# Kernel tuning notes

Measured on AMD Instinct MI355X. Metric: run time of the kernel, lower is better.

## Reference

```python
import jax, jax.numpy as jnp
import numpy as np

H, C = 8, 32          # heads, per-head channels
N, E = 100000, 1600000
NEG_SLOPE = 0.2
LN_EPS = 1e-5


def layer_norm(x, g, b):
    mu = jnp.mean(x, axis=-1, keepdims=True)
    var = jnp.mean((x - mu) ** 2, axis=-1, keepdims=True)
    return (x - mu) * jax.lax.rsqrt(var + LN_EPS) * g + b


def setup_inputs() -> dict:
    key = jax.random.key(0)
    ks = jax.random.split(key, 8)
    x = jax.random.normal(ks[0], (N, C), dtype=jnp.float32)
    edge_index = jax.random.randint(ks[1], (2, E), 0, N, dtype=jnp.int64)
    s = 1.0 / np.sqrt(C)
    W_gat = jax.random.normal(ks[2], (C, H * C), dtype=jnp.float32) * s
    att_src = jax.random.normal(ks[3], (H, C), dtype=jnp.float32) * s
    att_dst = jax.random.normal(ks[4], (H, C), dtype=jnp.float32) * s
    bias_gat = jnp.zeros((C,), jnp.float32)
    w1 = jax.random.normal(ks[5], (C, 128), dtype=jnp.float32) * s
    b1 = jnp.zeros((128,), jnp.float32)
    w2 = jax.random.normal(ks[6], (128, C), dtype=jnp.float32) / np.sqrt(128)
    b2 = jnp.zeros((C,), jnp.float32)
    g1 = jnp.ones((C,), jnp.float32); be1 = jnp.zeros((C,), jnp.float32)
    g2 = jnp.ones((C,), jnp.float32); be2 = jnp.zeros((C,), jnp.float32)
    return dict(x=x, edge_index=edge_index, W_gat=W_gat, att_src=att_src,
                att_dst=att_dst, bias_gat=bias_gat, w1=w1, b1=b1, w2=w2,
                b2=b2, g1=g1, be1=be1, g2=g2, be2=be2)


def gat_conv(x, edge_index, W_gat, att_src, att_dst, bias_gat):
    n = x.shape[0]
    # add self loops (PyG default)
    loops = jnp.arange(n, dtype=edge_index.dtype)
    ei = jnp.concatenate([edge_index, jnp.stack([loops, loops])], axis=1)
    src, dst = ei[0], ei[1]
    xp = (x @ W_gat).reshape(n, H, C)                      # [N,H,C]
    a_src = jnp.einsum('nhc,hc->nh', xp, att_src)          # [N,H]
    a_dst = jnp.einsum('nhc,hc->nh', xp, att_dst)
    alpha = jax.nn.leaky_relu(a_src[src] + a_dst[dst], NEG_SLOPE)  # [E',H]
    # segment softmax over incoming edges of each dst node
    m = jax.ops.segment_max(alpha, dst, num_segments=n)
    ea = jnp.exp(alpha - m[dst])
    denom = jax.ops.segment_sum(ea, dst, num_segments=n)
    attn = ea / (denom[dst] + 1e-16)                       # [E',H]
    msg = xp[src] * attn[..., None]                        # [E',H,C]
    out = jax.ops.segment_sum(msg, dst, num_segments=n)    # [N,H,C]
    return out.mean(axis=1) + bias_gat                     # concat=False -> head mean


def reference(x, edge_index, W_gat, att_src, att_dst, bias_gat,
              w1, b1, w2, b2, g1, be1, g2, be2):
    h = gat_conv(x, edge_index, W_gat, att_src, att_dst, bias_gat)
    h = layer_norm(h + x, g1, be1)
    ff = jax.nn.relu(h @ w1 + b1) @ w2 + b2
    return layer_norm(ff + h, g2, be2)
```

## Files before the change

### kernel.cpp

```cpp
#include <hip/hip_runtime.h>
#include <hip/hip_fp16.h>
#include <stdint.h>

#define HH 8
#define CC 32
#define HC 256
#define FF 128
#define NEG 0.2f
#define LNEPS 1e-5f

typedef __attribute__((ext_vector_type(8))) short bf16x8;
typedef __attribute__((ext_vector_type(4))) float f32x4;
typedef unsigned short u16;

__device__ inline unsigned bf16r(float f) {
  unsigned u = __float_as_uint(f);
  return (u + 0x7fffu + ((u >> 16) & 1u)) >> 16;
}
__device__ inline float bflo(unsigned w) { return __uint_as_float(w << 16); }
__device__ inline float bfhi(unsigned w) { return __uint_as_float(w & 0xffff0000u); }
__device__ inline float leaky(float v) { return v >= 0.f ? v : NEG * v; }
__device__ inline float h2f(unsigned hbits) {
  return __half2float(__ushort_as_half((unsigned short)hbits));
}
__device__ inline u16 f2h(float f) {
  return __half_as_ushort(__float2half(f));
}
__device__ inline float ub0(unsigned w) { return (float)(w & 0xffu); }
__device__ inline float ub1(unsigned w) { return (float)((w >> 8) & 0xffu); }
__device__ inline float ub2(unsigned w) { return (float)((w >> 16) & 0xffu); }
__device__ inline float ub3(unsigned w) { return (float)(w >> 24); }

__global__ __launch_bounds__(256) void klayout(
    const float* __restrict__ W, const float* __restrict__ atts,
    const float* __restrict__ attd, const float* __restrict__ w1,
    const float* __restrict__ w2,
    u16* __restrict__ Wb, u16* __restrict__ Zb,
    u16* __restrict__ V1b, u16* __restrict__ V2b, u16* __restrict__ WSb)
{
  int t0 = (int)blockIdx.x * 256 + (int)threadIdx.x;
  int st = (int)gridDim.x * 256;
  for (int i = t0; i < 16 * 512; i += st) {
    int j = i & 7, l = (i >> 3) & 63, nb = i >> 9;
    int k = 8 * (l >> 4) + j, c = 16 * nb + (l & 15);
    Wb[i] = (u16)bf16r(W[k * HC + c]);
  }
  for (int i = t0; i < 8 * 512; i += st) {
    int j = i & 7, l = (i >> 3) & 63, kb = i >> 9;
    int k = 32 * kb + 8 * (l >> 4) + j;
    int tc = l & 15;
    float v = 0.f;
    if (tc < 8)  { if ((k >> 5) == tc)     v = atts[tc * 32 + (k & 31)]; }
    else         { if ((k >> 5) == tc - 8) v = attd[(tc - 8) * 32 + (k & 31)]; }
    Zb[i] = (u16)bf16r(v);
  }
  for (int i = t0; i < 8 * 512; i += st) {
    int j = i & 7, l = (i >> 3) & 63, nb = i >> 9;
    int k = 8 * (l >> 4) + j, c = 16 * nb + (l & 15);
    V1b[i] = (u16)bf16r(w1[k * FF + c]);
  }
  for (int i = t0; i < 8 * 512; i += st) {
    int j = i & 7, l = (i >> 3) & 63, kn = i >> 9;
    int kb = kn >> 1, nb2 = kn & 1;
    int k = 32 * kb + 8 * (l >> 4) + j, c = 16 * nb2 + (l & 15);
    V2b[i] = (u16)bf16r(w2[k * CC + c]);
  }
  for (int i = t0; i < 16 * 512; i += st) {
    int j = i & 7, l = (i >> 3) & 63, kn = i >> 9;
    int kb = kn >> 1, nb2 = kn & 1;
    int krow = kb * 32 + 8 * (l >> 4) + j;
    int h = krow >> 5, kk = krow & 31;
    int c = 16 * nb2 + (l & 15);
    WSb[i] = (u16)bf16r(W[kk * HC + h * 32 + c]);
  }
}

__global__ __launch_bounds__(256) void k1c(
    const float* __restrict__ x, const u16* __restrict__ Wb,
    const u16* __restrict__ Zb, const int* __restrict__ ei,
    unsigned* __restrict__ xqx, unsigned* __restrict__ ascp,
    float* __restrict__ a_d, int* __restrict__ deg4,
    unsigned* __restrict__ dstr, int n, int e, int nbc)
{
  if ((int)blockIdx.x >= nbc) {
    int bi = (int)blockIdx.x - nbc;
    int r = bi & 3;
    int* dr = deg4 + (size_t)r * n;
    int i = bi * 1024 + (int)threadIdx.x * 4;
    if (i >= e) return;
    const int* dst = ei + e;
    if (i + 3 < e) {
      int4 d4 = *(const int4*)(dst + i);
      unsigned r0 = (unsigned)atomicAdd(&dr[d4.x], 1);
      unsigned r1 = (unsigned)atomicAdd(&dr[d4.y], 1);
      unsigned r2 = (unsigned)atomicAdd(&dr[d4.z], 1);
      unsigned r3 = (unsigned)atomicAdd(&dr[d4.w], 1);
      uint4 o;
      o.x = (unsigned)d4.x | ((unsigned)r << 17) | (r0 << 19);
      o.y = (unsigned)d4.y | ((unsigned)r << 17) | (r1 << 19);
      o.z = (unsigned)d4.z | ((unsigned)r << 17) | (r2 << 19);
      o.w = (unsigned)d4.w | ((unsigned)r << 17) | (r3 << 19);
      *(uint4*)(dstr + i) = o;
    } else {
      for (int k = 0; k < 4 && i + k < e; ++k) {
        int d = dst[i + k];
        unsigned rr = (unsigned)atomicAdd(&dr[d], 1);
        dstr[i + k] = (unsigned)d | ((unsigned)r << 17) | (rr << 19);
      }
    }
    return;
  }
  __shared__ u16 lt[4][16 * 264];
  int wid = threadIdx.x >> 6, lane = threadIdx.x & 63;
  int q = lane & 15, g = lane >> 4;
  long node0 = (long)((int)blockIdx.x * 4 + wid) * 16;
  if (node0 + 16 > n) node0 = n - 16;
  u16* L = lt[wid];
  u16* ascp16 = (u16*)ascp;

  const float* xr = x + (node0 + q) * CC + 8 * g;
  float4 xa = *(const float4*)xr, xb = *(const float4*)(xr + 4);
  bf16x8 af;
  af[0] = (short)bf16r(xa.x); af[1] = (short)bf16r(xa.y);
  af[2] = (short)bf16r(xa.z); af[3] = (short)bf16r(xa.w);
  af[4] = (short)bf16r(xb.x); af[5] = (short)bf16r(xb.y);
  af[6] = (short)bf16r(xb.z); af[7] = (short)bf16r(xb.w);

  float mx = fmaxf(fmaxf(fmaxf(fabsf(xa.x), fabsf(xa.y)), fmaxf(fabsf(xa.z), fabsf(xa.w))),
                   fmaxf(fmaxf(fabsf(xb.x), fabsf(xb.y)), fmaxf(fabsf(xb.z), fabsf(xb.w))));
  mx = fmaxf(mx, __shfl_xor(mx, 16));
  mx = fmaxf(mx, __shfl_xor(mx, 32));
  float rinv = (mx > 0.f) ? 127.f / mx : 0.f;
  u16 sch = f2h(mx * (1.f / 127.f));
  ascp16[((node0 + q) * HH + 2 * g) * 2 + 1]     = sch;
  ascp16[((node0 + q) * HH + 2 * g + 1) * 2 + 1] = sch;
  {
    int q0 = min(max(__float2int_rn(xa.x * rinv), -127), 127) + 128;
    int q1 = min(max(__float2int_rn(xa.y * rinv), -127), 127) + 128;
    int q2 = min(max(__float2int_rn(xa.z * rinv), -127), 127) + 128;
    int q3 = min(max(__float2int_rn(xa.w * rinv), -127), 127) + 128;
    int q4 = min(max(__float2int_rn(xb.x * rinv), -127), 127) + 128;
    int q5 = min(max(__float2int_rn(xb.y * rinv), -127), 127) + 128;
    int q6 = min(max(__float2int_rn(xb.z * rinv), -127), 127) + 128;
    int q7 = min(max(__float2int_rn(xb.w * rinv), -127), 127) + 128;
    uint2 pk;
    pk.x = (unsigned)q0 | ((unsigned)q1 << 8) | ((unsigned)q2 << 16) | ((unsigned)q3 << 24);
    pk.y = (unsigned)q4 | ((unsigned)q5 << 8) | ((unsigned)q6 << 16) | ((unsigned)q7 << 24);
    *(uint2*)(xqx + (node0 + q) * 8 + 2 * g) = pk;
  }

#pragma unroll
  for (int nb = 0; nb < 16; ++nb) {
    bf16x8 bf = *(const bf16x8*)(Wb + nb * 512 + lane * 8);
    f32x4 acc = {0.f, 0.f, 0.f, 0.f};
    acc = __builtin_amdgcn_mfma_f32_16x16x32_bf16(af, bf, acc, 0, 0, 0);
    int col = 16 * nb + q;
#pragma unroll
    for (int r = 0; r < 4; ++r)
      L[(4 * g + r) * 264 + col] = (u16)bf16r(acc[r]);
  }
  __syncthreads();

  f32x4 az = {0.f, 0.f, 0.f, 0.f};
#pragma unroll
  for (int kb = 0; kb < 8; ++kb) {
    bf16x8 a2 = *(const bf16x8*)(L + q * 264 + kb * 32 + g * 8);
    bf16x8 zb = *(const bf16x8*)(Zb + kb * 512 + lane * 8);
    az = __builtin_amdgcn_mfma_f32_16x16x32_bf16(a2, zb, az, 0, 0, 0);
  }
  int hq = q & 7;
  if (q < 8) {
#pragma unroll
    for (int r = 0; r < 4; ++r)
      ascp16[((node0 + 4 * g + r) * HH + hq) * 2] = (u16)bf16r(az[r]);
  } else {
#pragma unroll
    for (int r = 0; r < 4; ++r)
      a_d[(node0 + 4 * g + r) * HH + hq] = az[r];
  }
}

__global__ __launch_bounds__(256) void kscanA(const int* __restrict__ deg4,
                                              int* __restrict__ bsum, int n)
{
  __shared__ int ws[4];
  int t = threadIdx.x;
  int i = (int)blockIdx.x * 1024 + t * 4;
  int s = 0;
  if (i + 3 < n) {
#pragma unroll
    for (int r = 0; r < 4; ++r) {
      int4 v = *(const int4*)(deg4 + (size_t)r * n + i);
      s += v.x + v.y + v.z + v.w;
    }
  } else {
    for (int k = 0; k < 4 && i + k < n; ++k)
#pragma unroll
      for (int r = 0; r < 4; ++r) s += deg4[(size_t)r * n + i + k];
  }
#pragma unroll
  for (int mask = 1; mask < 64; mask <<= 1) s += __shfl_xor(s, mask);
  if ((t & 63) == 0) ws[t >> 6] = s;
  __syncthreads();
  if (t == 0) bsum[blockIdx.x] = ws[0] + ws[1] + ws[2] + ws[3];
}

__global__ __launch_bounds__(1024) void kscanB(int* __restrict__ bsum, int nb)
{
  __shared__ int wsum[16];
  int t = threadIdx.x, lane = t & 63, wid = t >> 6;
  int v = (t < nb) ? bsum[t] : 0;
  int s = v;
#pragma unroll
  for (int d = 1; d < 64; d <<= 1) { int tt = __shfl_up(s, d); if (lane >= d) s += tt; }
  if (lane == 63) wsum[wid] = s;
  __syncthreads();
  if (wid == 0) {
    int w = (lane < 16) ? wsum[lane] : 0;
#pragma unroll
    for (int d = 1; d < 16; d <<= 1) { int tt = __shfl_up(w, d); if (lane >= d) w += tt; }
    if (lane < 16) wsum[lane] = w;
  }
  __syncthreads();
  int excl = s - v + ((wid > 0) ? wsum[wid - 1] : 0);
  if (t < nb) bsum[t] = excl;
}

__global__ __launch_bounds__(256) void kscanC(const int* __restrict__ deg4,
                                              const int* __restrict__ bsum,
                                              int* __restrict__ rb,
                                              int* __restrict__ degt, int n)
{
  __shared__ int ws[4];
  int t = threadIdx.x, lane = t & 63, wid = t >> 6;
  int i = (int)blockIdx.x * 1024 + t * 4;
  int c0[4] = {0,0,0,0}, c1[4] = {0,0,0,0}, c2[4] = {0,0,0,0}, c3[4] = {0,0,0,0};
  if (i + 3 < n) {
    int4 v0 = *(const int4*)(deg4 + 0 * (size_t)n + i);
    int4 v1 = *(const int4*)(deg4 + 1 * (size_t)n + i);
    int4 v2 = *(const int4*)(deg4 + 2 * (size_t)n + i);
    int4 v3 = *(const int4*)(deg4 + 3 * (size_t)n + i);
    c0[0]=v0.x;c0[1]=v0.y;c0[2]=v0.z;c0[3]=v0.w;
    c1[0]=v1.x;c1[1]=v1.y;c1[2]=v1.z;c1[3]=v1.w;
    c2[0]=v2.x;c2[1]=v2.y;c2[2]=v2.z;c2[3]=v2.w;
    c3[0]=v3.x;c3[1]=v3.y;c3[2]=v3.z;c3[3]=v3.w;
  } else {
    for (int k = 0; k < 4 && i + k < n; ++k) {
      c0[k] = deg4[0 * (size_t)n + i + k];
      c1[k] = deg4[1 * (size_t)n + i + k];
      c2[k] = deg4[2 * (size_t)n + i + k];
      c3[k] = deg4[3 * (size_t)n + i + k];
    }
  }
  int tot[4];
#pragma unroll
  for (int k = 0; k < 4; ++k) tot[k] = c0[k] + c1[k] + c2[k] + c3[k];
  int tsum = tot[0] + tot[1] + tot[2] + tot[3];
  int s = tsum;
#pragma unroll
  for (int d = 1; d < 64; d <<= 1) { int tt = __shfl_up(s, d); if (lane >= d) s += tt; }
  if (lane == 63) ws[wid] = s;
  __syncthreads();
  if (t == 0) {
    int a = ws[0]; ws[0] = 0;
    int b = ws[1]; ws[1] = a; a += b;
    int c = ws[2]; ws[2] = a; a += c;
    ws[3] = a;
  }
  __syncthreads();
  int base = bsum[blockIdx.x] + ws[wid] + (s - tsum);
#pragma unroll
  for (int k = 0; k < 4; ++k) {
    if (i + k < n) {
      int b0 = base;
      rb[0 * (size_t)n + i + k] = b0;
      rb[1 * (size_t)n + i + k] = b0 + c0[k];
      rb[2 * (size_t)n + i + k] = b0 + c0[k] + c1[k];
      rb[3 * (size_t)n + i + k] = b0 + c0[k] + c1[k] + c2[k];
      degt[i + k] = tot[k];
    }
    base += tot[k];
  }
}

__global__ __launch_bounds__(256) void kscatter(
    const int* __restrict__ ei, const unsigned* __restrict__ dstr, int e,
    const int* __restrict__ rb, int* __restrict__ csr, int n)
{
  int oct = (int)blockIdx.x & 3;
  int nsub = (int)gridDim.x >> 2;
  int sub = (int)blockIdx.x >> 2;
  int nper = (n + 3) >> 2;
  int lo = oct * nper, hi = lo + nper;
  int stride = nsub << 10;
  for (int i = (sub * 256 + (int)threadIdx.x) * 4; i < e; i += stride) {
    if (i + 3 < e) {
      uint4 d4 = *(const uint4*)(dstr + i);
      int4 s4 = *(const int4*)(ei + i);
      int dx = d4.x & 0x1ffff, dy = d4.y & 0x1ffff,
          dz = d4.z & 0x1ffff, dw = d4.w & 0x1ffff;
      if (dx >= lo && dx < hi)
        csr[rb[(size_t)((d4.x >> 17) & 3) * n + dx] + (d4.x >> 19)] = s4.x;
      if (dy >= lo && dy < hi)
        csr[rb[(size_t)((d4.y >> 17) & 3) * n + dy] + (d4.y >> 19)] = s4.y;
      if (dz >= lo && dz < hi)
        csr[rb[(size_t)((d4.z >> 17) & 3) * n + dz] + (d4.z >> 19)] = s4.z;
      if (dw >= lo && dw < hi)
        csr[rb[(size_t)((d4.w >> 17) & 3) * n + dw] + (d4.w >> 19)] = s4.w;
    } else {
      for (int k = 0; k < 4 && i + k < e; ++k) {
        unsigned dv = dstr[i + k];
        int d = dv & 0x1ffff;
        if (d >= lo && d < hi)
          csr[rb[(size_t)((dv >> 17) & 3) * n + d] + (dv >> 19)] = ei[i + k];
      }
    }
  }
}

__global__ __launch_bounds__(256) void kagg(
    const int* __restrict__ csr, const int* __restrict__ offs,
    const int* __restrict__ degt,
    const unsigned* __restrict__ ascp, const float* __restrict__ a_d,
    const unsigned* __restrict__ xqx, unsigned* __restrict__ agg32, int n)
{
  int lane = threadIdx.x & 63;
  int wid  = threadIdx.x >> 6;
  int base = ((int)blockIdx.x * 4 + wid) * 4;
  int eg = lane >> 3, ha = lane & 7;
  int hb = eg;
  int c4 = lane & 7;

  for (int t = 0; t < 4; ++t) {
    int node = base + t;
    if (node >= n) return;
    int start = offs[node];
    int dg = degt[node];
    unsigned aw_self = ascp[(size_t)node * HH + ha];
    float ad_a  = a_d[(size_t)node * HH + ha];
    float aself = leaky(bflo(aw_self) + ad_a);

    float acc0 = 0.f, acc1 = 0.f, acc2 = 0.f, acc3 = 0.f;
    float dnA = 0.f, osA = 0.f;

    for (int j0 = 0; j0 < dg; j0 += 8) {
      int cnt = dg - j0; if (cnt > 8) cnt = 8;
      int idx = j0 + eg;
      int srcl = 0; float pw = 0.f;
      if (idx < dg) {
        srcl = csr[start + idx];
        unsigned av = ascp[(size_t)srcl * HH + ha];
        float al = leaky(bflo(av) + ad_a);
        float p  = __expf(al - aself);
        pw = p * h2f(av >> 16);
        dnA += p; osA += pw;
      }
      if (cnt == 8) {
#pragma unroll
        for (int j = 0; j < 8; ++j) {
          int sl = (j << 3) + hb;
          float wt = __shfl(pw, sl);
          int s = __shfl(srcl, sl);
          unsigned w = xqx[(size_t)s * 8 + c4];
          acc0 = fmaf(ub0(w), wt, acc0);
          acc1 = fmaf(ub1(w), wt, acc1);
          acc2 = fmaf(ub2(w), wt, acc2);
          acc3 = fmaf(ub3(w), wt, acc3);
        }
      } else {
        for (int j = 0; j < cnt; ++j) {
          int sl = (j << 3) + hb;
          float wt = __shfl(pw, sl);
          int s = __shfl(srcl, sl);
          unsigned w = xqx[(size_t)s * 8 + c4];
          acc0 = fmaf(ub0(w), wt, acc0);
          acc1 = fmaf(ub1(w), wt, acc1);
          acc2 = fmaf(ub2(w), wt, acc2);
          acc3 = fmaf(ub3(w), wt, acc3);
        }
      }
    }

    float dnH = dnA, osH = osA;
    dnH += __shfl_xor(dnH, 8);  osH += __shfl_xor(osH, 8);
    dnH += __shfl_xor(dnH, 16); osH += __shfl_xor(osH, 16);
    dnH += __shfl_xor(dnH, 32); osH += __shfl_xor(osH, 32);
    float dnB = __shfl(dnH, hb);
    float osB = __shfl(osH, hb);
    float scB = __shfl(h2f(aw_self >> 16), hb);

    {
      unsigned w = xqx[(size_t)node * 8 + c4];
      dnB += 1.f; osB += scB;
      acc0 = fmaf(ub0(w), scB, acc0);
      acc1 = fmaf(ub1(w), scB, acc1);
      acc2 = fmaf(ub2(w), scB, acc2);
      acc3 = fmaf(ub3(w), scB, acc3);
    }

    float corr = -128.f * osB;
    float inv = 0.125f / dnB;
    acc0 = (acc0 + corr) * inv;
    acc1 = (acc1 + corr) * inv;
    acc2 = (acc2 + corr) * inv;
    acc3 = (acc3 + corr) * inv;
    uint2 pk;
    pk.x = bf16r(acc0) | (bf16r(acc1) << 16);
    pk.y = bf16r(acc2) | (bf16r(acc3) << 16);
    *(uint2*)(agg32 + (size_t)node * 128 + hb * 16 + c4 * 2) = pk;
  }
}

__global__ __launch_bounds__(256) void k5m(
    const u16* __restrict__ agg16, const float* __restrict__ x,
    const float* __restrict__ bg, const u16* __restrict__ WSb,
    const u16* __restrict__ V1b, const u16* __restrict__ V2b,
    const float* __restrict__ b1, const float* __restrict__ b2,
    const float* __restrict__ g1, const float* __restrict__ be1,
    const float* __restrict__ g2, const float* __restrict__ be2,
    float* __restrict__ out, int n)
{
  __shared__ u16   lh[4][16 * 40];
  __shared__ u16   lf[4][16 * 136];
  __shared__ float lo[4][16 * 36];
  int wid = threadIdx.x >> 6, lane = threadIdx.x & 63;
  int q = lane & 15, g = lane >> 4;
  long node0 = (long)((int)blockIdx.x * 4 + wid) * 16;
  if (node0 + 16 > n) node0 = n - 16;
  u16* LH = lh[wid]; u16* LF = lf[wid]; float* LO = lo[wid];

  {
    int row = lane >> 2, off = (lane & 3) * 8;
    const float* x8 = x + (node0 + row) * CC + off;
    float4 c0 = *(const float4*)x8, c1 = *(const float4*)(x8 + 4);
    float4 bg0 = *(const float4*)(bg + off), bg1 = *(const float4*)(bg + off + 4);
    float4 s0 = make_float4(c0.x + bg0.x, c0.y + bg0.y, c0.z + bg0.z, c0.w + bg0.w);
    float4 s1 = make_float4(c1.x + bg1.x, c1.y + bg1.y, c1.z + bg1.z, c1.w + bg1.w);
    *(float4*)(LO + row * 36 + off)     = s0;
    *(float4*)(LO + row * 36 + off + 4) = s1;
  }
  __syncthreads();

  {
    f32x4 a20 = {0.f, 0.f, 0.f, 0.f}, a21 = {0.f, 0.f, 0.f, 0.f};
#pragma unroll
    for (int kb = 0; kb < 8; ++kb) {
      bf16x8 af = *(const bf16x8*)(agg16 + (node0 + q) * 256 + kb * 32 + g * 8);
      bf16x8 w0 = *(const bf16x8*)(WSb + (kb * 2 + 0) * 512 + lane * 8);
      bf16x8 w1v = *(const bf16x8*)(WSb + (kb * 2 + 1) * 512 + lane * 8);
      a20 = __builtin_amdgcn_mfma_f32_16x16x32_bf16(af, w0, a20, 0, 0, 0);
      a21 = __builtin_amdgcn_mfma_f32_16x16x32_bf16(af, w1v, a21, 0, 0, 0);
    }
#pragma unroll
    for (int r = 0; r < 4; ++r) {
      LO[(4 * g + r) * 36 + q]      += a20[r];
      LO[(4 * g + r) * 36 + 16 + q] += a21[r];
    }
  }
  __syncthreads();

  float hv[32];
  if (lane < 16) {
#pragma unroll
    for (int i = 0; i < 8; ++i) {
      float4 t = *(const float4*)(LO + q * 36 + i * 4);
      hv[4*i] = t.x; hv[4*i+1] = t.y; hv[4*i+2] = t.z; hv[4*i+3] = t.w;
    }
    float mu = 0.f;
#pragma unroll
    for (int c = 0; c < 32; ++c) mu += hv[c];
    mu *= (1.f / 32.f);
    float var = 0.f;
#pragma unroll
    for (int c = 0; c < 32; ++c) { float t = hv[c] - mu; var = fmaf(t, t, var); }
    float rs = rsqrtf(var * (1.f / 32.f) + LNEPS);
#pragma unroll
    for (int c = 0; c < 32; ++c) hv[c] = (hv[c] - mu) * rs * g1[c] + be1[c];
    uint* dst = (uint*)(LH + q * 40);
#pragma unroll
    for (int i = 0; i < 16; ++i)
      dst[i] = bf16r(hv[2*i]) | (bf16r(hv[2*i+1]) << 16);
  }
  __syncthreads();

  bf16x8 ah = *(const bf16x8*)(LH + q * 40 + g * 8);
#pragma unroll
  for (int nb = 0; nb < 8; ++nb) {
    bf16x8 v1 = *(const bf16x8*)(V1b + nb * 512 + lane * 8);
    f32x4 acc = {0.f, 0.f, 0.f, 0.f};
    acc = __builtin_amdgcn_mfma_f32_16x16x32_bf16(ah, v1, acc, 0, 0, 0);
    int col = 16 * nb + q;
    float bias = b1[col];
#pragma unroll
    for (int r = 0; r < 4; ++r) {
      float f = fmaxf(acc[r] + bias, 0.f);
      LF[(4 * g + r) * 136 + col] = (u16)bf16r(f);
    }
  }
  __syncthreads();

  f32x4 a20 = {0.f, 0.f, 0.f, 0.f}, a21 = {0.f, 0.f, 0.f, 0.f};
#pragma unroll
  for (int kb = 0; kb < 4; ++kb) {
    bf16x8 af2 = *(const bf16x8*)(LF + q * 136 + kb * 32 + g * 8);
    bf16x8 v20 = *(const bf16x8*)(V2b + (kb * 2 + 0) * 512 + lane * 8);
    bf16x8 v21 = *(const bf16x8*)(V2b + (kb * 2 + 1) * 512 + lane * 8);
    a20 = __builtin_amdgcn_mfma_f32_16x16x32_bf16(af2, v20, a20, 0, 0, 0);
    a21 = __builtin_amdgcn_mfma_f32_16x16x32_bf16(af2, v21, a21, 0, 0, 0);
  }
  __syncthreads();
#pragma unroll
  for (int r = 0; r < 4; ++r) {
    LO[(4 * g + r) * 36 + q]      = a20[r];
    LO[(4 * g + r) * 36 + 16 + q] = a21[r];
  }
  __syncthreads();

  if (lane < 16) {
    float ov[32];
#pragma unroll
    for (int i = 0; i < 8; ++i) {
      float4 t = *(const float4*)(LO + q * 36 + i * 4);
      ov[4*i] = t.x; ov[4*i+1] = t.y; ov[4*i+2] = t.z; ov[4*i+3] = t.w;
    }
#pragma unroll
    for (int c = 0; c < 32; ++c) ov[c] += b2[c] + hv[c];
    float mu2 = 0.f;
#pragma unroll
    for (int c = 0; c < 32; ++c) mu2 += ov[c];
    mu2 *= (1.f / 32.f);
    float var2 = 0.f;
#pragma unroll
    for (int c = 0; c < 32; ++c) { float t = ov[c] - mu2; var2 = fmaf(t, t, var2); }
    float rs2 = rsqrtf(var2 * (1.f / 32.f) + LNEPS);
    float* op = out + (node0 + q) * CC;
#pragma unroll
    for (int i = 0; i < 8; ++i) {
      float4 o;
      o.x = (ov[4*i]   - mu2) * rs2 * g2[4*i]   + be2[4*i];
      o.y = (ov[4*i+1] - mu2) * rs2 * g2[4*i+1] + be2[4*i+1];
      o.z = (ov[4*i+2] - mu2) * rs2 * g2[4*i+2] + be2[4*i+2];
      o.w = (ov[4*i+3] - mu2) * rs2 * g2[4*i+3] + be2[4*i+3];
      *(float4*)(op + i * 4) = o;
    }
  }
}

extern "C" void kernel_launch(void* const* d_in, const int* in_sizes, int n_in,
                              void* d_out, int out_size, void* d_ws, size_t ws_size,
                              hipStream_t stream)
{
  const float* x    = (const float*)d_in[0];
  const int*   ei   = (const int*)d_in[1];
  const float* W    = (const float*)d_in[2];
  const float* atts = (const float*)d_in[3];
  const float* attd = (const float*)d_in[4];
  const float* bg   = (const float*)d_in[5];
  const float* w1   = (const float*)d_in[6];
  const float* b1   = (const float*)d_in[7];
  const float* w2   = (const float*)d_in[8];
  const float* b2   = (const float*)d_in[9];
  const float* g1   = (const float*)d_in[10];
  const float* be1  = (const float*)d_in[11];
  const float* g2   = (const float*)d_in[12];
  const float* be2  = (const float*)d_in[13];

  int n = in_sizes[0] / CC;
  int e = in_sizes[1] / 2;

  uint8_t* ws = (uint8_t*)d_ws;
  size_t o = 0;
  unsigned* xqx = (unsigned*)(ws + o); o += (size_t)n * 32;
  unsigned* ascp = (unsigned*)(ws + o); o += (size_t)n * HH * 4;
  float* a_d = (float*)(ws + o); o += (size_t)n * HH * 4;
  unsigned* agg32 = (unsigned*)(ws + o); o += (size_t)n * 512;
  int* deg4   = (int*)(ws + o); o += (size_t)n * 4 * 4;
  int* rb     = (int*)(ws + o); o += (size_t)n * 4 * 4;
  int* degt   = (int*)(ws + o); o += (size_t)n * 4;
  unsigned* dstr = (unsigned*)(ws + o); o += (size_t)e * 4;
  int* csr    = (int*)(ws + o); o += (size_t)e * 4;
  int* bsum   = (int*)(ws + o); o += 4096;
  u16* Wb  = (u16*)(ws + o); o += 16 * 512 * 2;
  u16* Zb  = (u16*)(ws + o); o += 8 * 512 * 2;
  u16* V1b = (u16*)(ws + o); o += 8 * 512 * 2;
  u16* V2b = (u16*)(ws + o); o += 8 * 512 * 2;
  u16* WSb = (u16*)(ws + o); o += 16 * 512 * 2;

  (void)hipMemsetAsync(deg4, 0, (size_t)n * 4 * 4, stream);

  int nwaves = (n + 15) / 16;
  int nbc   = (nwaves + 3) / 4;
  int nb_e4 = (e + 1023) / 1024;
  int nb_s  = (n + 1023) / 1024;
  int nb_ag = (n + 15) / 16;

  klayout <<<16, 256, 0, stream>>>(W, atts, attd, w1, w2, Wb, Zb, V1b, V2b, WSb);
  k1c     <<<nbc + nb_e4, 256, 0, stream>>>(x, Wb, Zb, ei, xqx, ascp, a_d, deg4,
                                            dstr, n, e, nbc);
  kscanA  <<<nb_s, 256, 0, stream>>>(deg4, bsum, n);
  kscanB  <<<1, 1024, 0, stream>>>(bsum, nb_s);
  kscanC  <<<nb_s, 256, 0, stream>>>(deg4, bsum, rb, degt, n);
  kscatter<<<512, 256, 0, stream>>>(ei, dstr, e, rb, csr, n);
  kagg    <<<nb_ag, 256, 0, stream>>>(csr, rb, degt, ascp, a_d, xqx, agg32, n);
  k5m     <<<nbc, 256, 0, stream>>>((const u16*)agg32, x, bg, WSb, V1b, V2b,
                                    b1, b2, g1, be1, g2, be2, (float*)d_out, n);
}
```

Baseline: 231.1 us.

## Interleave per-node attention and quantized features into one 64-byte record; use 8 degree replicas

Merges the per-source attention/scale array and the int8 quantized feature array into a single 64-byte-per-node record. A gathered source in the aggregation kernel then touches one cache line instead of two. It also raises the number of degree-counter replicas from 4 to 8 to spread atomic contention in the edge counting pass, widening the rank field shift accordingly. In exchange the scan kernels read more replica rows and the rank field has one fewer bit.

```diff
diff --git a/kernel.cpp b/kernel.cpp
--- a/kernel.cpp
+++ b/kernel.cpp
@@ -8,6 +8,7 @@
 #define FF 128
 #define NEG 0.2f
 #define LNEPS 1e-5f
+#define NR 8
 
 typedef __attribute__((ext_vector_type(8))) short bf16x8;
 typedef __attribute__((ext_vector_type(4))) float f32x4;
@@ -78,14 +79,13 @@
 __global__ __launch_bounds__(256) void k1c(
     const float* __restrict__ x, const u16* __restrict__ Wb,
     const u16* __restrict__ Zb, const int* __restrict__ ei,
-    unsigned* __restrict__ xqx, unsigned* __restrict__ ascp,
-    float* __restrict__ a_d, int* __restrict__ deg4,
-    unsigned* __restrict__ dstr, int n, int e, int nbc)
+    unsigned* __restrict__ combo, float* __restrict__ a_d,
+    int* __restrict__ deg8, unsigned* __restrict__ dstr, int n, int e, int nbc)
 {
   if ((int)blockIdx.x >= nbc) {
     int bi = (int)blockIdx.x - nbc;
-    int r = bi & 3;
-    int* dr = deg4 + (size_t)r * n;
+    int r = bi & (NR - 1);
+    int* dr = deg8 + (size_t)r * n;
     int i = bi * 1024 + (int)threadIdx.x * 4;
     if (i >= e) return;
     const int* dst = ei + e;
@@ -96,16 +96,16 @@
       unsigned r2 = (unsigned)atomicAdd(&dr[d4.z], 1);
       unsigned r3 = (unsigned)atomicAdd(&dr[d4.w], 1);
       uint4 o;
-      o.x = (unsigned)d4.x | ((unsigned)r << 17) | (r0 << 19);
-      o.y = (unsigned)d4.y | ((unsigned)r << 17) | (r1 << 19);
-      o.z = (unsigned)d4.z | ((unsigned)r << 17) | (r2 << 19);
-      o.w = (unsigned)d4.w | ((unsigned)r << 17) | (r3 << 19);
+      o.x = (unsigned)d4.x | ((unsigned)r << 17) | (r0 << 20);
+      o.y = (unsigned)d4.y | ((unsigned)r << 17) | (r1 << 20);
+      o.z = (unsigned)d4.z | ((unsigned)r << 17) | (r2 << 20);
+      o.w = (unsigned)d4.w | ((unsigned)r << 17) | (r3 << 20);
       *(uint4*)(dstr + i) = o;
     } else {
       for (int k = 0; k < 4 && i + k < e; ++k) {
         int d = dst[i + k];
         unsigned rr = (unsigned)atomicAdd(&dr[d], 1);
-        dstr[i + k] = (unsigned)d | ((unsigned)r << 17) | (rr << 19);
+        dstr[i + k] = (unsigned)d | ((unsigned)r << 17) | (rr << 20);
       }
     }
     return;
@@ -116,7 +116,7 @@
   long node0 = (long)((int)blockIdx.x * 4 + wid) * 16;
   if (node0 + 16 > n) node0 = n - 16;
   u16* L = lt[wid];
-  u16* ascp16 = (u16*)ascp;
+  u16* combo16 = (u16*)combo;
 
   const float* xr = x + (node0 + q) * CC + 8 * g;
   float4 xa = *(const float4*)xr, xb = *(const float4*)(xr + 4);
@@ -132,8 +132,8 @@
   mx = fmaxf(mx, __shfl_xor(mx, 32));
   float rinv = (mx > 0.f) ? 127.f / mx : 0.f;
   u16 sch = f2h(mx * (1.f / 127.f));
-  ascp16[((node0 + q) * HH + 2 * g) * 2 + 1]     = sch;
-  ascp16[((node0 + q) * HH + 2 * g + 1) * 2 + 1] = sch;
+  combo16[((node0 + q) * 16 + 2 * g) * 2 + 1]     = sch;
+  combo16[((node0 + q) * 16 + 2 * g + 1) * 2 + 1] = sch;
   {
     int q0 = min(max(__float2int_rn(xa.x * rinv), -127), 127) + 128;
     int q1 = min(max(__float2int_rn(xa.y * rinv), -127), 127) + 128;
@@ -146,7 +146,7 @@
     uint2 pk;
     pk.x = (unsigned)q0 | ((unsigned)q1 << 8) | ((unsigned)q2 << 16) | ((unsigned)q3 << 24);
     pk.y = (unsigned)q4 | ((unsigned)q5 << 8) | ((unsigned)q6 << 16) | ((unsigned)q7 << 24);
-    *(uint2*)(xqx + (node0 + q) * 8 + 2 * g) = pk;
+    *(uint2*)(combo + (node0 + q) * 16 + 8 + 2 * g) = pk;
   }
 
 #pragma unroll
@@ -172,7 +172,7 @@
   if (q < 8) {
 #pragma unroll
     for (int r = 0; r < 4; ++r)
-      ascp16[((node0 + 4 * g + r) * HH + hq) * 2] = (u16)bf16r(az[r]);
+      combo16[((node0 + 4 * g + r) * 16 + hq) * 2] = (u16)bf16r(az[r]);
   } else {
 #pragma unroll
     for (int r = 0; r < 4; ++r)
@@ -180,7 +180,7 @@
   }
 }
 
-__global__ __launch_bounds__(256) void kscanA(const int* __restrict__ deg4,
+__global__ __launch_bounds__(256) void kscanA(const int* __restrict__ deg8,
                                               int* __restrict__ bsum, int n)
 {
   __shared__ int ws[4];
@@ -189,14 +189,14 @@
   int s = 0;
   if (i + 3 < n) {
 #pragma unroll
-    for (int r = 0; r < 4; ++r) {
-      int4 v = *(const int4*)(deg4 + (size_t)r * n + i);
+    for (int r = 0; r < NR; ++r) {
+      int4 v = *(const int4*)(deg8 + (size_t)r * n + i);
       s += v.x + v.y + v.z + v.w;
     }
   } else {
     for (int k = 0; k < 4 && i + k < n; ++k)
 #pragma unroll
-      for (int r = 0; r < 4; ++r) s += deg4[(size_t)r * n + i + k];
+      for (int r = 0; r < NR; ++r) s += deg8[(size_t)r * n + i + k];
   }
 #pragma unroll
   for (int mask = 1; mask < 64; mask <<= 1) s += __shfl_xor(s, mask);
@@ -226,7 +226,7 @@
   if (t < nb) bsum[t] = excl;
 }
 
-__global__ __launch_bounds__(256) void kscanC(const int* __restrict__ deg4,
+__global__ __launch_bounds__(256) void kscanC(const int* __restrict__ deg8,
                                               const int* __restrict__ bsum,
                                               int* __restrict__ rb,
                                               int* __restrict__ degt, int n)
@@ -234,27 +234,25 @@
   __shared__ int ws[4];
   int t = threadIdx.x, lane = t & 63, wid = t >> 6;
   int i = (int)blockIdx.x * 1024 + t * 4;
-  int c0[4] = {0,0,0,0}, c1[4] = {0,0,0,0}, c2[4] = {0,0,0,0}, c3[4] = {0,0,0,0};
-  if (i + 3 < n) {
-    int4 v0 = *(const int4*)(deg4 + 0 * (size_t)n + i);
-    int4 v1 = *(const int4*)(deg4 + 1 * (size_t)n + i);
-    int4 v2 = *(const int4*)(deg4 + 2 * (size_t)n + i);
-    int4 v3 = *(const int4*)(deg4 + 3 * (size_t)n + i);
-    c0[0]=v0.x;c0[1]=v0.y;c0[2]=v0.z;c0[3]=v0.w;
-    c1[0]=v1.x;c1[1]=v1.y;c1[2]=v1.z;c1[3]=v1.w;
-    c2[0]=v2.x;c2[1]=v2.y;c2[2]=v2.z;c2[3]=v2.w;
-    c3[0]=v3.x;c3[1]=v3.y;c3[2]=v3.z;c3[3]=v3.w;
-  } else {
-    for (int k = 0; k < 4 && i + k < n; ++k) {
-      c0[k] = deg4[0 * (size_t)n + i + k];
-      c1[k] = deg4[1 * (size_t)n + i + k];
-      c2[k] = deg4[2 * (size_t)n + i + k];
-      c3[k] = deg4[3 * (size_t)n + i + k];
+  int cr[NR][4];
+#pragma unroll
+  for (int r = 0; r < NR; ++r) {
+    if (i + 3 < n) {
+      int4 v = *(const int4*)(deg8 + (size_t)r * n + i);
+      cr[r][0] = v.x; cr[r][1] = v.y; cr[r][2] = v.z; cr[r][3] = v.w;
+    } else {
+      for (int k = 0; k < 4; ++k)
+        cr[r][k] = (i + k < n) ? deg8[(size_t)r * n + i + k] : 0;
     }
   }
   int tot[4];
 #pragma unroll
-  for (int k = 0; k < 4; ++k) tot[k] = c0[k] + c1[k] + c2[k] + c3[k];
+  for (int k = 0; k < 4; ++k) {
+    int s = 0;
+#pragma unroll
+    for (int r = 0; r < NR; ++r) s += cr[r][k];
+    tot[k] = s;
+  }
   int tsum = tot[0] + tot[1] + tot[2] + tot[3];
   int s = tsum;
 #pragma unroll
@@ -273,10 +271,11 @@
   for (int k = 0; k < 4; ++k) {
     if (i + k < n) {
       int b0 = base;
-      rb[0 * (size_t)n + i + k] = b0;
-      rb[1 * (size_t)n + i + k] = b0 + c0[k];
-      rb[2 * (size_t)n + i + k] = b0 + c0[k] + c1[k];
-      rb[3 * (size_t)n + i + k] = b0 + c0[k] + c1[k] + c2[k];
+#pragma unroll
+      for (int r = 0; r < NR; ++r) {
+        rb[(size_t)r * n + i + k] = b0;
+        b0 += cr[r][k];
+      }
       degt[i + k] = tot[k];
     }
     base += tot[k];
@@ -300,19 +299,19 @@
       int dx = d4.x & 0x1ffff, dy = d4.y & 0x1ffff,
           dz = d4.z & 0x1ffff, dw = d4.w & 0x1ffff;
       if (dx >= lo && dx < hi)
-        csr[rb[(size_t)((d4.x >> 17) & 3) * n + dx] + (d4.x >> 19)] = s4.x;
+        csr[rb[(size_t)((d4.x >> 17) & 7) * n + dx] + (d4.x >> 20)] = s4.x;
       if (dy >= lo && dy < hi)
-        csr[rb[(size_t)((d4.y >> 17) & 3) * n + dy] + (d4.y >> 19)] = s4.y;
+        csr[rb[(size_t)((d4.y >> 17) & 7) * n + dy] + (d4.y >> 20)] = s4.y;
       if (dz >= lo && dz < hi)
-        csr[rb[(size_t)((d4.z >> 17) & 3) * n + dz] + (d4.z >> 19)] = s4.z;
+        csr[rb[(size_t)((d4.z >> 17) & 7) * n + dz] + (d4.z >> 20)] = s4.z;
       if (dw >= lo && dw < hi)
-        csr[rb[(size_t)((d4.w >> 17) & 3) * n + dw] + (d4.w >> 19)] = s4.w;
+        csr[rb[(size_t)((d4.w >> 17) & 7) * n + dw] + (d4.w >> 20)] = s4.w;
     } else {
       for (int k = 0; k < 4 && i + k < e; ++k) {
         unsigned dv = dstr[i + k];
         int d = dv & 0x1ffff;
         if (d >= lo && d < hi)
-          csr[rb[(size_t)((dv >> 17) & 3) * n + d] + (dv >> 19)] = ei[i + k];
+          csr[rb[(size_t)((dv >> 17) & 7) * n + d] + (dv >> 20)] = ei[i + k];
       }
     }
   }
@@ -321,8 +320,8 @@
 __global__ __launch_bounds__(256) void kagg(
     const int* __restrict__ csr, const int* __restrict__ offs,
     const int* __restrict__ degt,
-    const unsigned* __restrict__ ascp, const float* __restrict__ a_d,
-    const unsigned* __restrict__ xqx, unsigned* __restrict__ agg32, int n)
+    const unsigned* __restrict__ combo, const float* __restrict__ a_d,
+    unsigned* __restrict__ agg32, int n)
 {
   int lane = threadIdx.x & 63;
   int wid  = threadIdx.x >> 6;
@@ -336,7 +335,7 @@
     if (node >= n) return;
     int start = offs[node];
     int dg = degt[node];
-    unsigned aw_self = ascp[(size_t)node * HH + ha];
+    unsigned aw_self = combo[(size_t)node * 16 + ha];
     float ad_a  = a_d[(size_t)node * HH + ha];
     float aself = leaky(bflo(aw_self) + ad_a);
 
@@ -349,7 +348,7 @@
       int srcl = 0; float pw = 0.f;
       if (idx < dg) {
         srcl = csr[start + idx];
-        unsigned av = ascp[(size_t)srcl * HH + ha];
+        unsigned av = combo[(size_t)srcl * 16 + ha];
         float al = leaky(bflo(av) + ad_a);
         float p  = __expf(al - aself);
         pw = p * h2f(av >> 16);
@@ -361,7 +360,7 @@
           int sl = (j << 3) + hb;
           float wt = __shfl(pw, sl);
           int s = __shfl(srcl, sl);
-          unsigned w = xqx[(size_t)s * 8 + c4];
+          unsigned w = combo[(size_t)s * 16 + 8 + c4];
           acc0 = fmaf(ub0(w), wt, acc0);
           acc1 = fmaf(ub1(w), wt, acc1);
           acc2 = fmaf(ub2(w), wt, acc2);
@@ -372,7 +371,7 @@
           int sl = (j << 3) + hb;
           float wt = __shfl(pw, sl);
           int s = __shfl(srcl, sl);
-          unsigned w = xqx[(size_t)s * 8 + c4];
+          unsigned w = combo[(size_t)s * 16 + 8 + c4];
           acc0 = fmaf(ub0(w), wt, acc0);
           acc1 = fmaf(ub1(w), wt, acc1);
           acc2 = fmaf(ub2(w), wt, acc2);
@@ -390,7 +389,7 @@
     float scB = __shfl(h2f(aw_self >> 16), hb);
 
     {
-      unsigned w = xqx[(size_t)node * 8 + c4];
+      unsigned w = combo[(size_t)node * 16 + 8 + c4];
       dnB += 1.f; osB += scB;
       acc0 = fmaf(ub0(w), scB, acc0);
       acc1 = fmaf(ub1(w), scB, acc1);
@@ -570,12 +569,11 @@
 
   uint8_t* ws = (uint8_t*)d_ws;
   size_t o = 0;
-  unsigned* xqx = (unsigned*)(ws + o); o += (size_t)n * 32;
-  unsigned* ascp = (unsigned*)(ws + o); o += (size_t)n * HH * 4;
+  unsigned* combo = (unsigned*)(ws + o); o += (size_t)n * 64;
   float* a_d = (float*)(ws + o); o += (size_t)n * HH * 4;
   unsigned* agg32 = (unsigned*)(ws + o); o += (size_t)n * 512;
-  int* deg4   = (int*)(ws + o); o += (size_t)n * 4 * 4;
-  int* rb     = (int*)(ws + o); o += (size_t)n * 4 * 4;
+  int* deg8   = (int*)(ws + o); o += (size_t)n * NR * 4;
+  int* rb     = (int*)(ws + o); o += (size_t)n * NR * 4;
   int* degt   = (int*)(ws + o); o += (size_t)n * 4;
   unsigned* dstr = (unsigned*)(ws + o); o += (size_t)e * 4;
   int* csr    = (int*)(ws + o); o += (size_t)e * 4;
@@ -586,7 +584,7 @@
   u16* V2b = (u16*)(ws + o); o += 8 * 512 * 2;
   u16* WSb = (u16*)(ws + o); o += 16 * 512 * 2;
 
-  (void)hipMemsetAsync(deg4, 0, (size_t)n * 4 * 4, stream);
+  (void)hipMemsetAsync(deg8, 0, (size_t)n * NR * 4, stream);
 
   int nwaves = (n + 15) / 16;
   int nbc   = (nwaves + 3) / 4;
@@ -595,13 +593,13 @@
   int nb_ag = (n + 15) / 16;
 
   klayout <<<16, 256, 0, stream>>>(W, atts, attd, w1, w2, Wb, Zb, V1b, V2b, WSb);
-  k1c     <<<nbc + nb_e4, 256, 0, stream>>>(x, Wb, Zb, ei, xqx, ascp, a_d, deg4,
+  k1c     <<<nbc + nb_e4, 256, 0, stream>>>(x, Wb, Zb, ei, combo, a_d, deg8,
                                             dstr, n, e, nbc);
-  kscanA  <<<nb_s, 256, 0, stream>>>(deg4, bsum, n);
+  kscanA  <<<nb_s, 256, 0, stream>>>(deg8, bsum, n);
   kscanB  <<<1, 1024, 0, stream>>>(bsum, nb_s);
-  kscanC  <<<nb_s, 256, 0, stream>>>(deg4, bsum, rb, degt, n);
+  kscanC  <<<nb_s, 256, 0, stream>>>(deg8, bsum, rb, degt, n);
   kscatter<<<512, 256, 0, stream>>>(ei, dstr, e, rb, csr, n);
-  kagg    <<<nb_ag, 256, 0, stream>>>(csr, rb, degt, ascp, a_d, xqx, agg32, n);
+  kagg    <<<nb_ag, 256, 0, stream>>>(csr, rb, degt, combo, a_d, agg32, n);
   k5m     <<<nbc, 256, 0, stream>>>((const u16*)agg32, x, bg, WSb, V1b, V2b,
                                     b1, b2, g1, be1, g2, be2, (float*)d_out, n);
 }
```

Result: no change. 232.1 us (+0.4%).
